# Optimization experiments

Hardware: AMD Instinct MI355X
Metric: run time of the kernel (lower is better)

The kernel has to match this reference:

```python
import jax, jax.numpy as jnp
import numpy as np

N, E, D, L = 100000, 500000, 128, 5
NUM_ATOM_FEATS, ATOM_VOCAB = 9, 120
NUM_BOND_FEATS, BOND_VOCAB = 3, 8
BN_EPS = 1e-5


def setup_inputs() -> dict:
    key = jax.random.key(0)
    ks = jax.random.split(key, 16)
    inp = {
        "x": jax.random.randint(ks[0], (N, NUM_ATOM_FEATS), 0, ATOM_VOCAB),
        "edge_index": jax.random.randint(ks[1], (2, E), 0, N),
        "edge_attr": jax.random.randint(ks[2], (E, NUM_BOND_FEATS), 0, BOND_VOCAB),
        "edge_weight": jax.random.uniform(ks[3], (E,), dtype=jnp.float32),
        # parameters
        "atom_emb": jax.random.normal(ks[4], (NUM_ATOM_FEATS, ATOM_VOCAB, D), dtype=jnp.float32) * 0.02,
        "bond_emb": jax.random.normal(ks[5], (L, NUM_BOND_FEATS, BOND_VOCAB, D), dtype=jnp.float32) * 0.02,
        "eps": jnp.zeros((L,), dtype=jnp.float32),
        "W1": jax.random.normal(ks[6], (L, D, 2 * D), dtype=jnp.float32) / np.sqrt(D),
        "b1": jnp.zeros((L, 2 * D), dtype=jnp.float32),
        "g1": jnp.ones((L, 2 * D), dtype=jnp.float32),
        "bt1": jnp.zeros((L, 2 * D), dtype=jnp.float32),
        "W2": jax.random.normal(ks[7], (L, 2 * D, D), dtype=jnp.float32) / np.sqrt(2 * D),
        "b2": jnp.zeros((L, D), dtype=jnp.float32),
        "g_out": jnp.ones((L, D), dtype=jnp.float32),
        "bt_out": jnp.zeros((L, D), dtype=jnp.float32),
    }
    return inp


def _batchnorm(h, g, b):
    # training-mode BN over node axis, biased variance (matches torch BN normalization)
    mu = jnp.mean(h, axis=0)
    var = jnp.mean((h - mu) ** 2, axis=0)
    return g * (h - mu) * jax.lax.rsqrt(var + BN_EPS) + b


def reference(x, edge_index, edge_attr, edge_weight,
              atom_emb, bond_emb, eps, W1, b1, g1, bt1, W2, b2, g_out, bt_out):
    # AtomEncoder: sum per-column embedding lookups -> [N, D]
    h = atom_emb[jnp.arange(NUM_ATOM_FEATS)[None, :], x].sum(axis=1)
    src, dst = edge_index[0], edge_index[1]
    ew = edge_weight[:, None]
    for l in range(L):
        # BondEncoder for layer l -> [E, D]
        e = bond_emb[l][jnp.arange(NUM_BOND_FEATS)[None, :], edge_attr].sum(axis=1)
        # message: relu(x_j + edge_emb) * edge_weight ; aggregate: scatter-add at dst
        m = jax.nn.relu(h[src] + e) * ew
        agg = jax.ops.segment_sum(m, dst, num_segments=N)
        z = (1.0 + eps[l]) * h + agg
        # GIN MLP: Linear -> BN -> ReLU -> Linear
        z = jax.nn.relu(_batchnorm(z @ W1[l] + b1[l], g1[l], bt1[l])) @ W2[l] + b2[l]
        # outer BatchNorm; dropout is identity in eval mode
        h_new = _batchnorm(z, g_out[l], bt_out[l])
        h = h_new if l == L - 1 else jax.nn.relu(h_new)
    return h
```

## Files before the change

### kernel.cpp

```cpp
#include <hip/hip_runtime.h>
#include <hip/hip_bf16.h>
#include <hip/hip_fp16.h>

#define NN 100000
#define EE 500000
#define NP 100096

typedef _Float16 f16;
typedef __attribute__((ext_vector_type(8))) _Float16 f16x8;
typedef __attribute__((ext_vector_type(4))) _Float16 f16x4;
typedef __attribute__((ext_vector_type(4))) float f32x4;

static __device__ __forceinline__ f16x8 relu8(f16x8 a) {
#if __has_builtin(__builtin_elementwise_max)
  f16x8 z = {0, 0, 0, 0, 0, 0, 0, 0};
  return __builtin_elementwise_max(a, z);
#else
  f16x8 r;
#pragma unroll
  for (int i = 0; i < 8; ++i) r[i] = (a[i] > (f16)0) ? a[i] : (f16)0;
  return r;
#endif
}

__global__ __launch_bounds__(256) void init_kernel(const float* __restrict__ W1,
                                                   const float* __restrict__ W2,
                                                   f16* __restrict__ w1f,
                                                   f16* __restrict__ w2f,
                                                   int* __restrict__ deg,
                                                   float* __restrict__ slices,
                                                   int* __restrict__ dmeta) {
  int gid = blockIdx.x * 256 + threadIdx.x;
  if (gid < 163840) {
    int l = gid / 32768; int rem = gid % 32768;
    int k = rem / 256;   int n = rem % 256;
    int ctg = n >> 4, m = n & 15;
    int c = k >> 5, q = (k >> 3) & 3, e = k & 7;
    int lane = q * 16 + m;
    w1f[l * 32768 + ((ctg * 4 + c) * 64 + lane) * 8 + e] = (f16)W1[gid];
  } else if (gid < 327680) {
    int g = gid - 163840;
    int l = g / 32768; int rem = g % 32768;
    int k = rem / 128; int n = rem % 128;
    int ctg = n >> 4, m = n & 15;
    int c = k >> 5, q = (k >> 3) & 3, e = k & 7;
    int lane = q * 16 + m;
    w2f[l * 32768 + ((ctg * 8 + c) * 64 + lane) * 8 + e] = (f16)W2[g];
  } else if (gid < 427680) {
    int i = gid - 327680;
    if (i < NN) deg[i] = 0;
  } else if (gid < 439968) {
    slices[gid - 427680] = 0.f;
  } else if (gid < 440096) {
    dmeta[gid - 439968] = 0;
  }
}

__global__ __launch_bounds__(256) void bondtab_kernel(const float* __restrict__ bemb,
                                                      f16* __restrict__ tab) {
  int gid = blockIdx.x * 256 + threadIdx.x;
  int l = gid >> 16;
  int rem = gid & 65535;
  int combo = rem >> 7, d = rem & 127;
  int a0 = combo & 7, a1 = (combo >> 3) & 7, a2 = combo >> 6;
  const float* bl = bemb + l * 3072;
  float v = bl[a0 * 128 + d] + bl[1024 + a1 * 128 + d] + bl[2048 + a2 * 128 + d];
  tab[gid] = (f16)v;
}

__global__ __launch_bounds__(256) void hist_kernel(const int* __restrict__ ei, int* __restrict__ deg) {
  int e = blockIdx.x * 256 + threadIdx.x;
  if (e < EE) atomicAdd(&deg[ei[EE + e]], 1);
}

__global__ __launch_bounds__(256) void scan1_kernel(const int* __restrict__ deg,
                                                    int* __restrict__ offs,
                                                    int* __restrict__ bsum) {
  __shared__ int sh[256];
  int b = blockIdx.x, t = threadIdx.x;
  int base = b * 1024 + t * 4;
  int v[4];
  int s = 0;
#pragma unroll
  for (int i = 0; i < 4; ++i) { v[i] = (base + i < NN) ? deg[base + i] : 0; s += v[i]; }
  sh[t] = s;
  __syncthreads();
  for (int off = 1; off < 256; off <<= 1) {
    int x = (t >= off) ? sh[t - off] : 0;
    __syncthreads();
    sh[t] += x;
    __syncthreads();
  }
  int excl = sh[t] - s;
  if (t == 255) bsum[b] = sh[255];
  int run = excl;
#pragma unroll
  for (int i = 0; i < 4; ++i) {
    if (base + i < NN) offs[base + i] = run;
    run += v[i];
  }
}

__global__ void scan2_kernel(int* __restrict__ bsum, int nb) {
  if (threadIdx.x == 0 && blockIdx.x == 0) {
    int run = 0;
    for (int i = 0; i < nb; ++i) { int v = bsum[i]; bsum[i] = run; run += v; }
  }
}

__global__ __launch_bounds__(256) void scan3_kernel(int* __restrict__ offs,
                                                    const int* __restrict__ bsum,
                                                    int* __restrict__ cursor) {
  int i = blockIdx.x * 256 + threadIdx.x;
  if (i < NN) {
    int v = offs[i] + bsum[i >> 10];
    offs[i] = v;
    cursor[i] = v;
  } else if (i == NN) {
    offs[NN] = EE;
  }
}

__global__ __launch_bounds__(256) void scatter_kernel(const int* __restrict__ ei,
                                                      const int* __restrict__ ea,
                                                      const float* __restrict__ ew,
                                                      int* __restrict__ cursor,
                                                      int2* __restrict__ pkw) {
  int e = blockIdx.x * 256 + threadIdx.x;
  if (e >= EE) return;
  int dst = ei[EE + e];
  int pos = atomicAdd(&cursor[dst], 1);
  int src = ei[e];
  int a0 = ea[e * 3 + 0], a1 = ea[e * 3 + 1], a2 = ea[e * 3 + 2];
  pkw[pos] = make_int2(src | (a0 << 17) | (a1 << 20) | (a2 << 23), __float_as_int(ew[e]));
}

__global__ __launch_bounds__(256) void dhist_kernel(const int* __restrict__ deg,
                                                    int* __restrict__ dhist) {
  __shared__ int lh[64];
  int t = threadIdx.x;
  if (t < 64) lh[t] = 0;
  __syncthreads();
  int n = blockIdx.x * 256 + t;
  if (n < NN) {
    int d = deg[n]; if (d > 63) d = 63;
    atomicAdd(&lh[d], 1);
  }
  __syncthreads();
  if (t < 64 && lh[t] > 0) atomicAdd(&dhist[t], lh[t]);
}

__global__ void dscan_kernel(const int* __restrict__ dhist, int* __restrict__ dcur) {
  if (threadIdx.x == 0 && blockIdx.x == 0) {
    int run = 0;
    for (int i = 0; i < 64; ++i) { int v = dhist[i]; dcur[i] = run; run += v; }
  }
}

__global__ __launch_bounds__(256) void dscatter_kernel(const int* __restrict__ deg,
                                                       int* __restrict__ dcur,
                                                       int* __restrict__ norder) {
  __shared__ int lcnt[64], lbase[64];
  int t = threadIdx.x;
  if (t < 64) lcnt[t] = 0;
  __syncthreads();
  int n = blockIdx.x * 256 + t;
  int b = 0, lpos = 0;
  bool valid = (n < NN);
  if (valid) {
    b = deg[n]; if (b > 63) b = 63;
    lpos = atomicAdd(&lcnt[b], 1);
  }
  __syncthreads();
  if (t < 64 && lcnt[t] > 0) lbase[t] = atomicAdd(&dcur[t], lcnt[t]);
  __syncthreads();
  if (valid) norder[lbase[b] + lpos] = n;
}

__global__ __launch_bounds__(256) void atom_kernel(const int* __restrict__ x,
                                                   const float* __restrict__ aemb,
                                                   f16* __restrict__ hf) {
  int gid = blockIdx.x * 256 + threadIdx.x;
  int n = gid >> 5, qq = gid & 31;
  if (n >= NN) return;
  float4 s = {0.f, 0.f, 0.f, 0.f};
#pragma unroll
  for (int f = 0; f < 9; ++f) {
    int xi = x[n * 9 + f];
    float4 v = *(const float4*)(aemb + (f * 120 + xi) * 128 + qq * 4);
    s.x += v.x; s.y += v.y; s.z += v.z; s.w += v.w;
  }
  f16x4 o;
  o[0] = (f16)s.x; o[1] = (f16)s.y; o[2] = (f16)s.z; o[3] = (f16)s.w;
  *(f16x4*)(hf + (long)n * 128 + qq * 4) = o;
}

__global__ __launch_bounds__(256) void edge_agg_kernel(const int* __restrict__ offs,
                                                       const int2* __restrict__ pkw,
                                                       const f16* __restrict__ tab,
                                                       const float* __restrict__ eps,
                                                       const int* __restrict__ norder,
                                                       const f16* __restrict__ hf,
                                                       f16* __restrict__ zb) {
  int gid = blockIdx.x * 256 + threadIdx.x;
  int g = gid >> 4, d0 = (gid & 15) * 8;
  if (g >= NN) {
    f16x8 z = {0, 0, 0, 0, 0, 0, 0, 0};
    *(f16x8*)(zb + (long)g * 128 + d0) = z;
    return;
  }
  int n = norder[g];
  int s0 = offs[n], s1 = offs[n + 1];
  float e1 = 1.f + eps[0];
  f16x8 hn = *(const f16x8*)(hf + (long)n * 128 + d0);
  float acc[8];
#pragma unroll
  for (int i = 0; i < 8; ++i) acc[i] = e1 * (float)hn[i];

  float wA, wB; f16x8 hA, bA, hB, bB;
  if (s0 < s1) {
    int2 pw = pkw[s0]; wA = __int_as_float(pw.y);
    hA = *(const f16x8*)(hf + (long)(pw.x & 131071) * 128 + d0);
    bA = *(const f16x8*)(tab + ((pw.x >> 17) & 511) * 128 + d0);
  }
  if (s0 + 1 < s1) {
    int2 pw = pkw[s0 + 1]; wB = __int_as_float(pw.y);
    hB = *(const f16x8*)(hf + (long)(pw.x & 131071) * 128 + d0);
    bB = *(const f16x8*)(tab + ((pw.x >> 17) & 511) * 128 + d0);
  }
  int e = s0;
  for (; e + 1 < s1; e += 2) {
    {
      f16x8 sm = relu8(hA + bA);
#pragma unroll
      for (int i = 0; i < 8; ++i) acc[i] += (float)sm[i] * wA;
      if (e + 2 < s1) {
        int2 pw = pkw[e + 2]; wA = __int_as_float(pw.y);
        hA = *(const f16x8*)(hf + (long)(pw.x & 131071) * 128 + d0);
        bA = *(const f16x8*)(tab + ((pw.x >> 17) & 511) * 128 + d0);
      }
    }
    {
      f16x8 sm = relu8(hB + bB);
#pragma unroll
      for (int i = 0; i < 8; ++i) acc[i] += (float)sm[i] * wB;
      if (e + 3 < s1) {
        int2 pw = pkw[e + 3]; wB = __int_as_float(pw.y);
        hB = *(const f16x8*)(hf + (long)(pw.x & 131071) * 128 + d0);
        bB = *(const f16x8*)(tab + ((pw.x >> 17) & 511) * 128 + d0);
      }
    }
  }
  if (e < s1) {
    f16x8 sm = relu8(hA + bA);
#pragma unroll
    for (int i = 0; i < 8; ++i) acc[i] += (float)sm[i] * wA;
  }
  f16x8 o;
#pragma unroll
  for (int i = 0; i < 8; ++i) o[i] = (f16)acc[i];
  *(f16x8*)(zb + (long)n * 128 + d0) = o;
}

__global__ __launch_bounds__(256) void edge_agg_bn_kernel(const int* __restrict__ offs,
                                                          const int2* __restrict__ pkw,
                                                          const f16* __restrict__ tab,
                                                          const float* __restrict__ eps, int l,
                                                          const int* __restrict__ norder,
                                                          const f16* __restrict__ t2,
                                                          const float* __restrict__ sum2s,
                                                          const float* __restrict__ sq2s,
                                                          const float* __restrict__ g2,
                                                          const float* __restrict__ bt2,
                                                          float* __restrict__ s1z,
                                                          f16* __restrict__ zb) {
  __shared__ float sc2[128], sh2[128];
  const int tid = threadIdx.x;
  if (tid < 128) {
    float s = 0.f, s2 = 0.f;
#pragma unroll
    for (int k = 0; k < 16; ++k) { s += sum2s[k * 128 + tid]; s2 += sq2s[k * 128 + tid]; }
    float mu = s * (1.f / NN);
    float var = fmaxf(s2 * (1.f / NN) - mu * mu, 0.f);
    float is = rsqrtf(var + 1e-5f);
    float sc = g2[tid] * is;
    sc2[tid] = sc;
    sh2[tid] = bt2[tid] - mu * sc;
  }
  if (blockIdx.x == 0) {
#pragma unroll
    for (int j = 0; j < 8; ++j)
      *(float4*)(s1z + (j * 256 + tid) * 4) = float4{0.f, 0.f, 0.f, 0.f};
  }
  __syncthreads();
  int gid = blockIdx.x * 256 + tid;
  int g = gid >> 4, d0 = (gid & 15) * 8;
  if (g >= NN) {
    f16x8 z = {0, 0, 0, 0, 0, 0, 0, 0};
    *(f16x8*)(zb + (long)g * 128 + d0) = z;
    return;
  }
  int n = norder[g];
  float4 svA = *(const float4*)(sc2 + d0), svB = *(const float4*)(sc2 + d0 + 4);
  float4 shA = *(const float4*)(sh2 + d0), shB = *(const float4*)(sh2 + d0 + 4);
  float sv[8] = {svA.x, svA.y, svA.z, svA.w, svB.x, svB.y, svB.z, svB.w};
  float hv[8] = {shA.x, shA.y, shA.z, shA.w, shB.x, shB.y, shB.z, shB.w};
  f16x8 sv8, hv8;
#pragma unroll
  for (int i = 0; i < 8; ++i) { sv8[i] = (f16)sv[i]; hv8[i] = (f16)hv[i]; }

  int s0 = offs[n], s1 = offs[n + 1];
  float e1 = 1.f + eps[l];
  f16x8 hn = *(const f16x8*)(t2 + (long)n * 128 + d0);
  float acc[8];
#pragma unroll
  for (int i = 0; i < 8; ++i)
    acc[i] = e1 * fmaxf((float)hn[i] * sv[i] + hv[i], 0.f);

  float wA, wB; f16x8 hA, bA, hB, bB;
  if (s0 < s1) {
    int2 pw = pkw[s0]; wA = __int_as_float(pw.y);
    hA = *(const f16x8*)(t2 + (long)(pw.x & 131071) * 128 + d0);
    bA = *(const f16x8*)(tab + ((pw.x >> 17) & 511) * 128 + d0);
  }
  if (s0 + 1 < s1) {
    int2 pw = pkw[s0 + 1]; wB = __int_as_float(pw.y);
    hB = *(const f16x8*)(t2 + (long)(pw.x & 131071) * 128 + d0);
    bB = *(const f16x8*)(tab + ((pw.x >> 17) & 511) * 128 + d0);
  }
  int e = s0;
  for (; e + 1 < s1; e += 2) {
    {
      f16x8 y = relu8(hA * sv8 + hv8);
      f16x8 sm = relu8(y + bA);
#pragma unroll
      for (int i = 0; i < 8; ++i) acc[i] += (float)sm[i] * wA;
      if (e + 2 < s1) {
        int2 pw = pkw[e + 2]; wA = __int_as_float(pw.y);
        hA = *(const f16x8*)(t2 + (long)(pw.x & 131071) * 128 + d0);
        bA = *(const f16x8*)(tab + ((pw.x >> 17) & 511) * 128 + d0);
      }
    }
    {
      f16x8 y = relu8(hB * sv8 + hv8);
      f16x8 sm = relu8(y + bB);
#pragma unroll
      for (int i = 0; i < 8; ++i) acc[i] += (float)sm[i] * wB;
      if (e + 3 < s1) {
        int2 pw = pkw[e + 3]; wB = __int_as_float(pw.y);
        hB = *(const f16x8*)(t2 + (long)(pw.x & 131071) * 128 + d0);
        bB = *(const f16x8*)(tab + ((pw.x >> 17) & 511) * 128 + d0);
      }
    }
  }
  if (e < s1) {
    f16x8 y = relu8(hA * sv8 + hv8);
    f16x8 sm = relu8(y + bA);
#pragma unroll
    for (int i = 0; i < 8; ++i) acc[i] += (float)sm[i] * wA;
  }
  f16x8 o;
#pragma unroll
  for (int i = 0; i < 8; ++i) o[i] = (f16)acc[i];
  *(f16x8*)(zb + (long)n * 128 + d0) = o;
}

__global__ __launch_bounds__(256) void gemm1_kernel(const f16* __restrict__ zb,
                                                    const f16* __restrict__ w1f,
                                                    f16* __restrict__ t1f,
                                                    float* __restrict__ sum1s,
                                                    float* __restrict__ sq1s,
                                                    float* __restrict__ s2z) {
  __shared__ __align__(16) char ldsraw[17408];
  const int tid = threadIdx.x;
  const int lane = tid & 63, w = tid >> 6;
  const int wr = w >> 1, wc = w & 1;
  const int m = lane & 15, q = lane >> 4;
  const int cb = blockIdx.x;
  const int rbase = blockIdx.y * 64;
  const int slice = blockIdx.y & 15;

  if (blockIdx.y == 0 && cb == 0) {
#pragma unroll
    for (int j = 0; j < 4; ++j)
      *(float4*)(s2z + (j * 256 + tid) * 4) = float4{0.f, 0.f, 0.f, 0.f};
  }

  f16x8 B[4][4];
#pragma unroll
  for (int ct = 0; ct < 4; ++ct)
#pragma unroll
    for (int c = 0; c < 4; ++c)
      B[ct][c] = *(const f16x8*)(w1f + (((cb * 8 + wc * 4 + ct) * 4 + c) * 64 + lane) * 8);

  {
    f16x8 st[4];
    const int tofs = tid * 16;
#pragma unroll
    for (int j = 0; j < 4; ++j)
      st[j] = *(const f16x8*)(zb + (long)rbase * 128 + (tofs + j * 4096) / 2);
#pragma unroll
    for (int j = 0; j < 4; ++j) {
      int ofs = tofs + j * 4096;
      int row = ofs >> 8, colb = ofs & 255;
      *(f16x8*)(ldsraw + row * 256 + (colb ^ ((row & 7) << 4))) = st[j];
    }
  }
  __syncthreads();

  f16x8 A[2][4];
#pragma unroll
  for (int rt = 0; rt < 2; ++rt) {
    int row = wr * 32 + rt * 16 + m;
    int rs = row * 256, sw = (row & 7) << 4;
#pragma unroll
    for (int c = 0; c < 4; ++c) {
      int colb = c * 64 + q * 16;
      A[rt][c] = *(const f16x8*)(ldsraw + rs + (colb ^ sw));
    }
  }

  f32x4 acc[2][4];
  const f32x4 zf = {0.f, 0.f, 0.f, 0.f};
#pragma unroll
  for (int a = 0; a < 2; ++a)
#pragma unroll
    for (int b = 0; b < 4; ++b) acc[a][b] = zf;

#pragma unroll
  for (int c = 0; c < 4; ++c)
#pragma unroll
    for (int rt = 0; rt < 2; ++rt)
#pragma unroll
      for (int ct = 0; ct < 4; ++ct)
        acc[rt][ct] = __builtin_amdgcn_mfma_f32_16x16x32_f16(A[rt][c], B[ct][c], acc[rt][ct], 0, 0, 0);

  __syncthreads();
  f16 (*sh)[136] = (f16(*)[136])ldsraw;

#pragma unroll
  for (int ct = 0; ct < 4; ++ct) {
    int lc = wc * 64 + ct * 16 + m;
    int gc = cb * 128 + lc;
    float s = 0.f, s2 = 0.f;
#pragma unroll
    for (int rt = 0; rt < 2; ++rt) {
      int lr = wr * 32 + rt * 16 + q * 4;
#pragma unroll
      for (int i = 0; i < 4; ++i) {
        float v = acc[rt][ct][i];
        s += v; s2 += v * v;
        sh[lr + i][lc] = (f16)v;
      }
    }
    s  += __shfl_xor(s, 16);  s  += __shfl_xor(s, 32);
    s2 += __shfl_xor(s2, 16); s2 += __shfl_xor(s2, 32);
    if (q == 0) {
      unsafeAtomicAdd(&sum1s[slice * 256 + gc], s);
      unsafeAtomicAdd(&sq1s[slice * 256 + gc], s2);
    }
  }
  __syncthreads();
  const int colc = tid & 15, r0 = tid >> 4;
#pragma unroll
  for (int j = 0; j < 4; ++j) {
    int r = j * 16 + r0;
    f16x8 v = *(const f16x8*)(&sh[r][colc * 8]);
    *(f16x8*)(t1f + (long)(rbase + r) * 256 + cb * 128 + colc * 8) = v;
  }
}

__global__ __launch_bounds__(256) void gemm2_kernel(const f16* __restrict__ a1,
                                                    const f16* __restrict__ w2f,
                                                    const float* __restrict__ sum1s,
                                                    const float* __restrict__ sq1s,
                                                    const float* __restrict__ g1,
                                                    const float* __restrict__ bt1,
                                                    f16* __restrict__ t2out,
                                                    float* __restrict__ sum2s,
                                                    float* __restrict__ sq2s) {
  __shared__ __align__(16) char ldsraw[34816];
  float* sc1 = (float*)(ldsraw + 32768);
  float* sh1 = (float*)(ldsraw + 33792);
  const int tid = threadIdx.x;
  const int lane = tid & 63, w = tid >> 6;
  const int wr = w >> 1, wc = w & 1;
  const int m = lane & 15, q = lane >> 4;
  const int rbase = blockIdx.x * 64;
  const int slice = blockIdx.x & 15;

  f16x8 st[8];
  const int tofs = tid * 16;
#pragma unroll
  for (int j = 0; j < 8; ++j)
    st[j] = *(const f16x8*)(a1 + (long)rbase * 256 + (tofs + j * 4096) / 2);

  {
    float s = 0.f, s2 = 0.f;
#pragma unroll
    for (int k = 0; k < 16; ++k) { s += sum1s[k * 256 + tid]; s2 += sq1s[k * 256 + tid]; }
    float mu = s * (1.f / NN);
    float var = fmaxf(s2 * (1.f / NN) - mu * mu, 0.f);
    float is = rsqrtf(var + 1e-5f);
    float sc = g1[tid] * is;
    sc1[tid] = sc;
    sh1[tid] = bt1[tid] - mu * sc;
  }
  __syncthreads();

  {
    const int k0 = (tid & 31) * 8;
    float4 sa = *(const float4*)(sc1 + k0);
    float4 sb = *(const float4*)(sc1 + k0 + 4);
    float4 ha = *(const float4*)(sh1 + k0);
    float4 hb = *(const float4*)(sh1 + k0 + 4);
#pragma unroll
    for (int j = 0; j < 8; ++j) {
      int ofs = tofs + j * 4096;
      int row = ofs >> 9, colb = ofs & 511;
      f16x8 u = st[j], o;
      o[0] = (f16)fmaxf((float)u[0] * sa.x + ha.x, 0.f);
      o[1] = (f16)fmaxf((float)u[1] * sa.y + ha.y, 0.f);
      o[2] = (f16)fmaxf((float)u[2] * sa.z + ha.z, 0.f);
      o[3] = (f16)fmaxf((float)u[3] * sa.w + ha.w, 0.f);
      o[4] = (f16)fmaxf((float)u[4] * sb.x + hb.x, 0.f);
      o[5] = (f16)fmaxf((float)u[5] * sb.y + hb.y, 0.f);
      o[6] = (f16)fmaxf((float)u[6] * sb.z + hb.z, 0.f);
      o[7] = (f16)fmaxf((float)u[7] * sb.w + hb.w, 0.f);
      *(f16x8*)(ldsraw + row * 512 + (colb ^ ((row & 7) << 4))) = o;
    }
  }
  __syncthreads();

  f32x4 acc[2][4];
  const f32x4 zf = {0.f, 0.f, 0.f, 0.f};
#pragma unroll
  for (int a = 0; a < 2; ++a)
#pragma unroll
    for (int b = 0; b < 4; ++b) acc[a][b] = zf;

#pragma unroll
  for (int hh = 0; hh < 2; ++hh) {
    f16x8 A[2][4], B[4][4];
#pragma unroll
    for (int rt = 0; rt < 2; ++rt) {
      int row = wr * 32 + rt * 16 + m;
      int rs = row * 512, sw = (row & 7) << 4;
#pragma unroll
      for (int c = 0; c < 4; ++c) {
        int colb = (hh * 4 + c) * 64 + q * 16;
        A[rt][c] = *(const f16x8*)(ldsraw + rs + (colb ^ sw));
      }
    }
#pragma unroll
    for (int ct = 0; ct < 4; ++ct)
#pragma unroll
      for (int c = 0; c < 4; ++c)
        B[ct][c] = *(const f16x8*)(w2f + (((wc * 4 + ct) * 8 + hh * 4 + c) * 64 + lane) * 8);
#pragma unroll
    for (int c = 0; c < 4; ++c)
#pragma unroll
      for (int rt = 0; rt < 2; ++rt)
#pragma unroll
        for (int ct = 0; ct < 4; ++ct)
          acc[rt][ct] = __builtin_amdgcn_mfma_f32_16x16x32_f16(A[rt][c], B[ct][c], acc[rt][ct], 0, 0, 0);
  }

  __syncthreads();
  f16 (*sh)[136] = (f16(*)[136])ldsraw;

#pragma unroll
  for (int ct = 0; ct < 4; ++ct) {
    int gc = wc * 64 + ct * 16 + m;
    float s = 0.f, s2 = 0.f;
#pragma unroll
    for (int rt = 0; rt < 2; ++rt) {
      int grow = rbase + wr * 32 + rt * 16 + q * 4;
      int lr = wr * 32 + rt * 16 + q * 4;
#pragma unroll
      for (int i = 0; i < 4; ++i) {
        float v = acc[rt][ct][i];
        float vv = (grow + i < NN) ? v : 0.f;
        s += vv; s2 += vv * vv;
        sh[lr + i][gc] = (f16)v;
      }
    }
    s  += __shfl_xor(s, 16);  s  += __shfl_xor(s, 32);
    s2 += __shfl_xor(s2, 16); s2 += __shfl_xor(s2, 32);
    if (q == 0) {
      unsafeAtomicAdd(&sum2s[slice * 128 + gc], s);
      unsafeAtomicAdd(&sq2s[slice * 128 + gc], s2);
    }
  }
  __syncthreads();
  const int colc = tid & 15, r0 = tid >> 4;
#pragma unroll
  for (int j = 0; j < 4; ++j) {
    int r = j * 16 + r0;
    f16x8 v = *(const f16x8*)(&sh[r][colc * 8]);
    *(f16x8*)(t2out + (long)(rbase + r) * 128 + colc * 8) = v;
  }
}

__global__ __launch_bounds__(256) void apply_kernel(const f16* __restrict__ t2,
                                                    const float* __restrict__ sum2s,
                                                    const float* __restrict__ sq2s,
                                                    const float* __restrict__ g2,
                                                    const float* __restrict__ bt2,
                                                    float* __restrict__ outp) {
  __shared__ float sc2[128], sh2[128];
  const int tid = threadIdx.x;
  if (tid < 128) {
    float s = 0.f, s2 = 0.f;
#pragma unroll
    for (int k = 0; k < 16; ++k) { s += sum2s[k * 128 + tid]; s2 += sq2s[k * 128 + tid]; }
    float mu = s * (1.f / NN);
    float var = fmaxf(s2 * (1.f / NN) - mu * mu, 0.f);
    float is = rsqrtf(var + 1e-5f);
    float sc = g2[tid] * is;
    sc2[tid] = sc;
    sh2[tid] = bt2[tid] - mu * sc;
  }
  __syncthreads();
  const int rbase = blockIdx.x * 64;
#pragma unroll
  for (int k = 0; k < 4; ++k) {
    int ci = tid + k * 256;
    int r = ci >> 4, c8 = ci & 15;
    int row = rbase + r;
    if (row >= NN) continue;
    f16x8 u = *(const f16x8*)(t2 + (long)row * 128 + c8 * 8);
    float4 sa = *(const float4*)(sc2 + c8 * 8);
    float4 sb = *(const float4*)(sc2 + c8 * 8 + 4);
    float4 ha = *(const float4*)(sh2 + c8 * 8);
    float4 hb = *(const float4*)(sh2 + c8 * 8 + 4);
    float4 o0 = {(float)u[0] * sa.x + ha.x, (float)u[1] * sa.y + ha.y,
                 (float)u[2] * sa.z + ha.z, (float)u[3] * sa.w + ha.w};
    float4 o1 = {(float)u[4] * sb.x + hb.x, (float)u[5] * sb.y + hb.y,
                 (float)u[6] * sb.z + hb.z, (float)u[7] * sb.w + hb.w};
    *(float4*)(outp + (long)row * 128 + c8 * 8) = o0;
    *(float4*)(outp + (long)row * 128 + c8 * 8 + 4) = o1;
  }
}

extern "C" void kernel_launch(void* const* d_in, const int* in_sizes, int n_in,
                              void* d_out, int out_size, void* d_ws, size_t ws_size,
                              hipStream_t stream) {
  (void)in_sizes; (void)n_in; (void)out_size; (void)ws_size;
  const int*   x      = (const int*)d_in[0];
  const int*   ei     = (const int*)d_in[1];
  const int*   ea     = (const int*)d_in[2];
  const float* ew     = (const float*)d_in[3];
  const float* aemb   = (const float*)d_in[4];
  const float* bemb   = (const float*)d_in[5];
  const float* eps    = (const float*)d_in[6];
  const float* W1     = (const float*)d_in[7];
  const float* g1     = (const float*)d_in[9];
  const float* bt1    = (const float*)d_in[10];
  const float* W2     = (const float*)d_in[11];
  const float* g_out  = (const float*)d_in[13];
  const float* bt_out = (const float*)d_in[14];

  float* outp = (float*)d_out;

  char* ws = (char*)d_ws;
  f16*   hf    = (f16*)(ws);
  f16*   zb    = (f16*)(ws + 25624576);
  f16*   t1f   = (f16*)(ws + 51249152);
  f16*   w1f   = (f16*)(ws + 102498304);
  f16*   w2f   = (f16*)(ws + 102825984);
  float* slices= (float*)(ws + 103153664);
  int*   offs  = (int*)(ws + 103202816);
  int*   bsum  = (int*)(ws + 103602848);
  int*   deg   = (int*)(ws + 103603360);
  int*   cursor= (int*)(ws + 104003360);
  f16*   bsumtab = (f16*)(ws + 103603360);
  int2*  pkw   = (int2*)(ws + 104403360);
  int*   norder= (int*)(ws + 108403360);
  int*   dmeta = (int*)(ws + 108803744);

  int* dhist = dmeta;
  int* dcur  = dmeta + 64;

  float* sum1s = slices;
  float* sq1s  = slices + 4096;
  float* sum2s = slices + 8192;
  float* sq2s  = slices + 10240;

  init_kernel<<<1720, 256, 0, stream>>>(W1, W2, w1f, w2f, deg, slices, dmeta);
  hist_kernel<<<1954, 256, 0, stream>>>(ei, deg);
  scan1_kernel<<<98, 256, 0, stream>>>(deg, offs, bsum);
  scan2_kernel<<<1, 64, 0, stream>>>(bsum, 98);
  scan3_kernel<<<392, 256, 0, stream>>>(offs, bsum, cursor);
  scatter_kernel<<<1954, 256, 0, stream>>>(ei, ea, ew, cursor, pkw);
  dhist_kernel<<<391, 256, 0, stream>>>(deg, dhist);
  dscan_kernel<<<1, 64, 0, stream>>>(dhist, dcur);
  dscatter_kernel<<<391, 256, 0, stream>>>(deg, dcur, norder);
  bondtab_kernel<<<1280, 256, 0, stream>>>(bemb, bsumtab);
  atom_kernel<<<12500, 256, 0, stream>>>(x, aemb, hf);

  for (int l = 0; l < 5; ++l) {
    if (l == 0) {
      edge_agg_kernel<<<6256, 256, 0, stream>>>(offs, pkw, bsumtab, eps, norder, hf, zb);
    } else {
      edge_agg_bn_kernel<<<6256, 256, 0, stream>>>(offs, pkw, bsumtab + l * 65536, eps, l,
                                                   norder, hf, sum2s, sq2s,
                                                   g_out + (l - 1) * 128, bt_out + (l - 1) * 128,
                                                   sum1s, zb);
    }
    gemm1_kernel<<<dim3(2, 1564), 256, 0, stream>>>(zb, w1f + l * 32768, t1f, sum1s, sq1s, sum2s);
    gemm2_kernel<<<1564, 256, 0, stream>>>(t1f, w2f + l * 32768, sum1s, sq1s,
                                           g1 + l * 256, bt1 + l * 256, hf, sum2s, sq2s);
    if (l == 4)
      apply_kernel<<<1564, 256, 0, stream>>>(hf, sum2s, sq2s, g_out + 512, bt_out + 512, outp);
  }
}
```

Before: 588.9 us.

## Fuse GIN MLP GEMMs into one persistent kernel with grid barrier

```diff
diff --git a/kernel.cpp b/kernel.cpp
--- a/kernel.cpp
+++ b/kernel.cpp
@@ -5,6 +5,8 @@
 #define NN 100000
 #define EE 500000
 #define NP 100096
+#define NTILE 1564
+#define NBLK 782
 
 typedef _Float16 f16;
 typedef __attribute__((ext_vector_type(8))) _Float16 f16x8;
@@ -51,7 +53,7 @@
     if (i < NN) deg[i] = 0;
   } else if (gid < 439968) {
     slices[gid - 427680] = 0.f;
-  } else if (gid < 440096) {
+  } else if (gid < 440104) {
     dmeta[gid - 439968] = 0;
   }
 }
@@ -365,135 +367,194 @@
   *(f16x8*)(zb + (long)n * 128 + d0) = o;
 }
 
-__global__ __launch_bounds__(256) void gemm1_kernel(const f16* __restrict__ zb,
-                                                    const f16* __restrict__ w1f,
-                                                    f16* __restrict__ t1f,
-                                                    float* __restrict__ sum1s,
-                                                    float* __restrict__ sq1s,
-                                                    float* __restrict__ s2z) {
-  __shared__ __align__(16) char ldsraw[17408];
+__device__ __forceinline__ void phaseA(int tile, const f16* __restrict__ zb,
+                                       const f16* __restrict__ w1f,
+                                       float* __restrict__ sum1s, float* __restrict__ sq1s,
+                                       char* lds, f16x8 (&H)[2][2][2]) {
   const int tid = threadIdx.x;
   const int lane = tid & 63, w = tid >> 6;
   const int wr = w >> 1, wc = w & 1;
   const int m = lane & 15, q = lane >> 4;
-  const int cb = blockIdx.x;
-  const int rbase = blockIdx.y * 64;
-  const int slice = blockIdx.y & 15;
-
-  if (blockIdx.y == 0 && cb == 0) {
-#pragma unroll
-    for (int j = 0; j < 4; ++j)
-      *(float4*)(s2z + (j * 256 + tid) * 4) = float4{0.f, 0.f, 0.f, 0.f};
-  }
-
-  f16x8 B[4][4];
-#pragma unroll
-  for (int ct = 0; ct < 4; ++ct)
-#pragma unroll
-    for (int c = 0; c < 4; ++c)
-      B[ct][c] = *(const f16x8*)(w1f + (((cb * 8 + wc * 4 + ct) * 4 + c) * 64 + lane) * 8);
-
-  {
-    f16x8 st[4];
-    const int tofs = tid * 16;
-#pragma unroll
-    for (int j = 0; j < 4; ++j)
-      st[j] = *(const f16x8*)(zb + (long)rbase * 128 + (tofs + j * 4096) / 2);
-#pragma unroll
-    for (int j = 0; j < 4; ++j) {
-      int ofs = tofs + j * 4096;
-      int row = ofs >> 8, colb = ofs & 255;
-      *(f16x8*)(ldsraw + row * 256 + (colb ^ ((row & 7) << 4))) = st[j];
-    }
-  }
-  __syncthreads();
-
-  f16x8 A[2][4];
-#pragma unroll
-  for (int rt = 0; rt < 2; ++rt) {
-    int row = wr * 32 + rt * 16 + m;
-    int rs = row * 256, sw = (row & 7) << 4;
+  const long rbase = (long)tile * 64;
+  const int slice = tile & 15;
+  f16x8 st[4];
+  const int tofs = tid * 16;
+#pragma unroll
+  for (int j = 0; j < 4; ++j)
+    st[j] = *(const f16x8*)(zb + rbase * 128 + (tofs + j * 4096) / 2);
+  __syncthreads();
+#pragma unroll
+  for (int j = 0; j < 4; ++j) {
+    int ofs = tofs + j * 4096;
+    int row = ofs >> 8, colb = ofs & 255;
+    *(f16x8*)(lds + row * 256 + (colb ^ ((row & 7) << 4))) = st[j];
+  }
+  __syncthreads();
+  const int r0 = wr * 32 + m, r1 = wr * 32 + 16 + m;
+  const int sw = (m & 7) << 4;
+#pragma unroll
+  for (int h = 0; h < 2; ++h) {
+    f32x4 a0c[4], a1c[4];
+    const f32x4 zf = {0.f, 0.f, 0.f, 0.f};
+#pragma unroll
+    for (int ct = 0; ct < 4; ++ct) { a0c[ct] = zf; a1c[ct] = zf; }
 #pragma unroll
     for (int c = 0; c < 4; ++c) {
       int colb = c * 64 + q * 16;
-      A[rt][c] = *(const f16x8*)(ldsraw + rs + (colb ^ sw));
-    }
-  }
-
-  f32x4 acc[2][4];
-  const f32x4 zf = {0.f, 0.f, 0.f, 0.f};
-#pragma unroll
-  for (int a = 0; a < 2; ++a)
-#pragma unroll
-    for (int b = 0; b < 4; ++b) acc[a][b] = zf;
-
-#pragma unroll
-  for (int c = 0; c < 4; ++c)
-#pragma unroll
-    for (int rt = 0; rt < 2; ++rt)
-#pragma unroll
-      for (int ct = 0; ct < 4; ++ct)
-        acc[rt][ct] = __builtin_amdgcn_mfma_f32_16x16x32_f16(A[rt][c], B[ct][c], acc[rt][ct], 0, 0, 0);
-
-  __syncthreads();
-  f16 (*sh)[136] = (f16(*)[136])ldsraw;
-
-#pragma unroll
-  for (int ct = 0; ct < 4; ++ct) {
-    int lc = wc * 64 + ct * 16 + m;
-    int gc = cb * 128 + lc;
-    float s = 0.f, s2 = 0.f;
-#pragma unroll
-    for (int rt = 0; rt < 2; ++rt) {
-      int lr = wr * 32 + rt * 16 + q * 4;
+      f16x8 A0 = *(const f16x8*)(lds + r0 * 256 + (colb ^ sw));
+      f16x8 A1 = *(const f16x8*)(lds + r1 * 256 + (colb ^ sw));
+#pragma unroll
+      for (int ct = 0; ct < 4; ++ct) {
+        f16x8 B = *(const f16x8*)(w1f + (((h * 8 + wc * 4 + ct) * 4 + c) * 64 + lane) * 8);
+        a0c[ct] = __builtin_amdgcn_mfma_f32_16x16x32_f16(A0, B, a0c[ct], 0, 0, 0);
+        a1c[ct] = __builtin_amdgcn_mfma_f32_16x16x32_f16(A1, B, a1c[ct], 0, 0, 0);
+      }
+    }
+#pragma unroll
+    for (int ct = 0; ct < 4; ++ct) {
+      int gc = h * 128 + wc * 64 + ct * 16 + m;
+      float s = 0.f, s2 = 0.f;
 #pragma unroll
       for (int i = 0; i < 4; ++i) {
-        float v = acc[rt][ct][i];
-        s += v; s2 += v * v;
-        sh[lr + i][lc] = (f16)v;
-      }
-    }
-    s  += __shfl_xor(s, 16);  s  += __shfl_xor(s, 32);
-    s2 += __shfl_xor(s2, 16); s2 += __shfl_xor(s2, 32);
-    if (q == 0) {
-      unsafeAtomicAdd(&sum1s[slice * 256 + gc], s);
-      unsafeAtomicAdd(&sq1s[slice * 256 + gc], s2);
-    }
-  }
-  __syncthreads();
-  const int colc = tid & 15, r0 = tid >> 4;
-#pragma unroll
-  for (int j = 0; j < 4; ++j) {
-    int r = j * 16 + r0;
-    f16x8 v = *(const f16x8*)(&sh[r][colc * 8]);
-    *(f16x8*)(t1f + (long)(rbase + r) * 256 + cb * 128 + colc * 8) = v;
-  }
-}
-
-__global__ __launch_bounds__(256) void gemm2_kernel(const f16* __restrict__ a1,
-                                                    const f16* __restrict__ w2f,
-                                                    const float* __restrict__ sum1s,
-                                                    const float* __restrict__ sq1s,
-                                                    const float* __restrict__ g1,
-                                                    const float* __restrict__ bt1,
-                                                    f16* __restrict__ t2out,
-                                                    float* __restrict__ sum2s,
-                                                    float* __restrict__ sq2s) {
-  __shared__ __align__(16) char ldsraw[34816];
-  float* sc1 = (float*)(ldsraw + 32768);
-  float* sh1 = (float*)(ldsraw + 33792);
+        float v0 = a0c[ct][i], v1 = a1c[ct][i];
+        s += v0 + v1; s2 += v0 * v0 + v1 * v1;
+        H[h][0][(ct * 4 + i) >> 3][(ct * 4 + i) & 7] = (f16)v0;
+        H[h][1][(ct * 4 + i) >> 3][(ct * 4 + i) & 7] = (f16)v1;
+      }
+      s  += __shfl_xor(s, 16);  s  += __shfl_xor(s, 32);
+      s2 += __shfl_xor(s2, 16); s2 += __shfl_xor(s2, 32);
+      if (q == 0) {
+        unsafeAtomicAdd(&sum1s[slice * 256 + gc], s);
+        unsafeAtomicAdd(&sq1s[slice * 256 + gc], s2);
+      }
+    }
+  }
+}
+
+__device__ __forceinline__ void phaseB(int tile, const f16* __restrict__ w2f,
+                                       const float* scL, const float* shL,
+                                       float* __restrict__ sum2s, float* __restrict__ sq2s,
+                                       f16* __restrict__ t2out,
+                                       char* lds, f16x8 (&H)[2][2][2]) {
   const int tid = threadIdx.x;
   const int lane = tid & 63, w = tid >> 6;
   const int wr = w >> 1, wc = w & 1;
   const int m = lane & 15, q = lane >> 4;
-  const int rbase = blockIdx.x * 64;
-  const int slice = blockIdx.x & 15;
-
-  f16x8 st[8];
-  const int tofs = tid * 16;
-#pragma unroll
-  for (int j = 0; j < 8; ++j)
-    st[j] = *(const f16x8*)(a1 + (long)rbase * 256 + (tofs + j * 4096) / 2);
+  const long rbase = (long)tile * 64;
+  const int slice = tile & 15;
+  const int r0 = wr * 32 + m, r1 = wr * 32 + 16 + m;
+  const int sw = (m & 7) << 4;
+  f32x4 o0c[4], o1c[4];
+  const f32x4 zf = {0.f, 0.f, 0.f, 0.f};
+#pragma unroll
+  for (int ct = 0; ct < 4; ++ct) { o0c[ct] = zf; o1c[ct] = zf; }
+#pragma unroll
+  for (int h = 0; h < 2; ++h) {
+#pragma unroll
+    for (int rt = 0; rt < 2; ++rt) {
+#pragma unroll
+      for (int ct = 0; ct < 4; ++ct) {
+        int lc = wc * 64 + ct * 16 + m;
+        int gc = h * 128 + lc;
+        float sc = scL[gc], sh = shL[gc];
+#pragma unroll
+        for (int i = 0; i < 4; ++i) {
+          float v = (float)H[h][rt][(ct * 4 + i) >> 3][(ct * 4 + i) & 7];
+          int r = wr * 32 + rt * 16 + q * 4 + i;
+          *(f16*)(lds + r * 256 + ((2 * lc) ^ ((r & 7) << 4))) = (f16)fmaxf(v * sc + sh, 0.f);
+        }
+      }
+    }
+    __syncthreads();
+#pragma unroll
+    for (int c = 0; c < 4; ++c) {
+      int colb = c * 64 + q * 16;
+      f16x8 A0 = *(const f16x8*)(lds + r0 * 256 + (colb ^ sw));
+      f16x8 A1 = *(const f16x8*)(lds + r1 * 256 + (colb ^ sw));
+#pragma unroll
+      for (int ct = 0; ct < 4; ++ct) {
+        f16x8 B = *(const f16x8*)(w2f + (((wc * 4 + ct) * 8 + h * 4 + c) * 64 + lane) * 8);
+        o0c[ct] = __builtin_amdgcn_mfma_f32_16x16x32_f16(A0, B, o0c[ct], 0, 0, 0);
+        o1c[ct] = __builtin_amdgcn_mfma_f32_16x16x32_f16(A1, B, o1c[ct], 0, 0, 0);
+      }
+    }
+    __syncthreads();
+  }
+  f16 (*sh136)[136] = (f16(*)[136])lds;
+#pragma unroll
+  for (int ct = 0; ct < 4; ++ct) {
+    int gc = wc * 64 + ct * 16 + m;
+    float s = 0.f, s2 = 0.f;
+    long grow0 = rbase + wr * 32 + q * 4;
+    long grow1 = grow0 + 16;
+    int lr0 = wr * 32 + q * 4, lr1 = lr0 + 16;
+#pragma unroll
+    for (int i = 0; i < 4; ++i) {
+      float v = o0c[ct][i];
+      float vm = (grow0 + i < NN) ? v : 0.f;
+      s += vm; s2 += vm * vm;
+      sh136[lr0 + i][gc] = (f16)v;
+    }
+#pragma unroll
+    for (int i = 0; i < 4; ++i) {
+      float v = o1c[ct][i];
+      float vm = (grow1 + i < NN) ? v : 0.f;
+      s += vm; s2 += vm * vm;
+      sh136[lr1 + i][gc] = (f16)v;
+    }
+    s  += __shfl_xor(s, 16);  s  += __shfl_xor(s, 32);
+    s2 += __shfl_xor(s2, 16); s2 += __shfl_xor(s2, 32);
+    if (q == 0) {
+      unsafeAtomicAdd(&sum2s[slice * 128 + gc], s);
+      unsafeAtomicAdd(&sq2s[slice * 128 + gc], s2);
+    }
+  }
+  __syncthreads();
+  const int colc = tid & 15, rr = tid >> 4;
+#pragma unroll
+  for (int j = 0; j < 4; ++j) {
+    int r = j * 16 + rr;
+    f16x8 v = *(const f16x8*)(&sh136[r][colc * 8]);
+    *(f16x8*)(t2out + (rbase + r) * 128 + colc * 8) = v;
+  }
+  __syncthreads();
+}
+
+__global__ __launch_bounds__(256, 4) void gemm12_kernel(const f16* __restrict__ zb,
+                                                        const f16* __restrict__ w1f,
+                                                        const f16* __restrict__ w2f,
+                                                        const float* __restrict__ g1,
+                                                        const float* __restrict__ bt1,
+                                                        float* __restrict__ sum1s,
+                                                        float* __restrict__ sq1s,
+                                                        float* __restrict__ sum2s,
+                                                        f16* __restrict__ t2out,
+                                                        int* __restrict__ bar) {
+  __shared__ __align__(16) char lds[19456];
+  float* scL = (float*)(lds + 17408);
+  float* shL = (float*)(lds + 18432);
+  const int tid = threadIdx.x;
+  const int b = blockIdx.x;
+  const int t0v = 2 * b, t1v = 2 * b + 1;
+  f16x8 H0[2][2][2], H1[2][2][2];
+
+  if (b == 0) {
+#pragma unroll
+    for (int j = 0; j < 4; ++j)
+      *(float4*)(sum2s + (j * 256 + tid) * 4) = float4{0.f, 0.f, 0.f, 0.f};
+  }
+
+  phaseA(t0v, zb, w1f, sum1s, sq1s, lds, H0);
+  phaseA(t1v, zb, w1f, sum1s, sq1s, lds, H1);
+
+  __syncthreads();
+  if (tid == 0) {
+    __threadfence();
+    __hip_atomic_fetch_add(bar, 1, __ATOMIC_ACQ_REL, __HIP_MEMORY_SCOPE_AGENT);
+    while (__hip_atomic_load(bar, __ATOMIC_ACQUIRE, __HIP_MEMORY_SCOPE_AGENT) < NBLK)
+      __builtin_amdgcn_s_sleep(32);
+  }
+  __syncthreads();
 
   {
     float s = 0.f, s2 = 0.f;
@@ -503,103 +564,14 @@
     float var = fmaxf(s2 * (1.f / NN) - mu * mu, 0.f);
     float is = rsqrtf(var + 1e-5f);
     float sc = g1[tid] * is;
-    sc1[tid] = sc;
-    sh1[tid] = bt1[tid] - mu * sc;
-  }
-  __syncthreads();
-
-  {
-    const int k0 = (tid & 31) * 8;
-    float4 sa = *(const float4*)(sc1 + k0);
-    float4 sb = *(const float4*)(sc1 + k0 + 4);
-    float4 ha = *(const float4*)(sh1 + k0);
-    float4 hb = *(const float4*)(sh1 + k0 + 4);
-#pragma unroll
-    for (int j = 0; j < 8; ++j) {
-      int ofs = tofs + j * 4096;
-      int row = ofs >> 9, colb = ofs & 511;
-      f16x8 u = st[j], o;
-      o[0] = (f16)fmaxf((float)u[0] * sa.x + ha.x, 0.f);
-      o[1] = (f16)fmaxf((float)u[1] * sa.y + ha.y, 0.f);
-      o[2] = (f16)fmaxf((float)u[2] * sa.z + ha.z, 0.f);
-      o[3] = (f16)fmaxf((float)u[3] * sa.w + ha.w, 0.f);
-      o[4] = (f16)fmaxf((float)u[4] * sb.x + hb.x, 0.f);
-      o[5] = (f16)fmaxf((float)u[5] * sb.y + hb.y, 0.f);
-      o[6] = (f16)fmaxf((float)u[6] * sb.z + hb.z, 0.f);
-      o[7] = (f16)fmaxf((float)u[7] * sb.w + hb.w, 0.f);
-      *(f16x8*)(ldsraw + row * 512 + (colb ^ ((row & 7) << 4))) = o;
-    }
-  }
-  __syncthreads();
-
-  f32x4 acc[2][4];
-  const f32x4 zf = {0.f, 0.f, 0.f, 0.f};
-#pragma unroll
-  for (int a = 0; a < 2; ++a)
-#pragma unroll
-    for (int b = 0; b < 4; ++b) acc[a][b] = zf;
-
-#pragma unroll
-  for (int hh = 0; hh < 2; ++hh) {
-    f16x8 A[2][4], B[4][4];
-#pragma unroll
-    for (int rt = 0; rt < 2; ++rt) {
-      int row = wr * 32 + rt * 16 + m;
-      int rs = row * 512, sw = (row & 7) << 4;
-#pragma unroll
-      for (int c = 0; c < 4; ++c) {
-        int colb = (hh * 4 + c) * 64 + q * 16;
-        A[rt][c] = *(const f16x8*)(ldsraw + rs + (colb ^ sw));
-      }
-    }
-#pragma unroll
-    for (int ct = 0; ct < 4; ++ct)
-#pragma unroll
-      for (int c = 0; c < 4; ++c)
-        B[ct][c] = *(const f16x8*)(w2f + (((wc * 4 + ct) * 8 + hh * 4 + c) * 64 + lane) * 8);
-#pragma unroll
-    for (int c = 0; c < 4; ++c)
-#pragma unroll
-      for (int rt = 0; rt < 2; ++rt)
-#pragma unroll
-        for (int ct = 0; ct < 4; ++ct)
-          acc[rt][ct] = __builtin_amdgcn_mfma_f32_16x16x32_f16(A[rt][c], B[ct][c], acc[rt][ct], 0, 0, 0);
-  }
-
-  __syncthreads();
-  f16 (*sh)[136] = (f16(*)[136])ldsraw;
-
-#pragma unroll
-  for (int ct = 0; ct < 4; ++ct) {
-    int gc = wc * 64 + ct * 16 + m;
-    float s = 0.f, s2 = 0.f;
-#pragma unroll
-    for (int rt = 0; rt < 2; ++rt) {
-      int grow = rbase + wr * 32 + rt * 16 + q * 4;
-      int lr = wr * 32 + rt * 16 + q * 4;
-#pragma unroll
-      for (int i = 0; i < 4; ++i) {
-        float v = acc[rt][ct][i];
-        float vv = (grow + i < NN) ? v : 0.f;
-        s += vv; s2 += vv * vv;
-        sh[lr + i][gc] = (f16)v;
-      }
-    }
-    s  += __shfl_xor(s, 16);  s  += __shfl_xor(s, 32);
-    s2 += __shfl_xor(s2, 16); s2 += __shfl_xor(s2, 32);
-    if (q == 0) {
-      unsafeAtomicAdd(&sum2s[slice * 128 + gc], s);
-      unsafeAtomicAdd(&sq2s[slice * 128 + gc], s2);
-    }
-  }
-  __syncthreads();
-  const int colc = tid & 15, r0 = tid >> 4;
-#pragma unroll
-  for (int j = 0; j < 4; ++j) {
-    int r = j * 16 + r0;
-    f16x8 v = *(const f16x8*)(&sh[r][colc * 8]);
-    *(f16x8*)(t2out + (long)(rbase + r) * 128 + colc * 8) = v;
-  }
+    scL[tid] = sc;
+    shL[tid] = bt1[tid] - mu * sc;
+  }
+  __syncthreads();
+
+  float* sq2s = sum2s + 2048;
+  phaseB(t0v, w2f, scL, shL, sum2s, sq2s, t2out, lds, H0);
+  phaseB(t1v, w2f, scL, shL, sum2s, sq2s, t2out, lds, H1);
 }
 
 __global__ __launch_bounds__(256) void apply_kernel(const f16* __restrict__ t2,
@@ -666,7 +638,6 @@
   char* ws = (char*)d_ws;
   f16*   hf    = (f16*)(ws);
   f16*   zb    = (f16*)(ws + 25624576);
-  f16*   t1f   = (f16*)(ws + 51249152);
   f16*   w1f   = (f16*)(ws + 102498304);
   f16*   w2f   = (f16*)(ws + 102825984);
   float* slices= (float*)(ws + 103153664);
@@ -681,6 +652,7 @@
 
   int* dhist = dmeta;
   int* dcur  = dmeta + 64;
+  int* bar   = dmeta + 128;
 
   float* sum1s = slices;
   float* sq1s  = slices + 4096;
@@ -708,9 +680,9 @@
                                                    g_out + (l - 1) * 128, bt_out + (l - 1) * 128,
                                                    sum1s, zb);
     }
-    gemm1_kernel<<<dim3(2, 1564), 256, 0, stream>>>(zb, w1f + l * 32768, t1f, sum1s, sq1s, sum2s);
-    gemm2_kernel<<<1564, 256, 0, stream>>>(t1f, w2f + l * 32768, sum1s, sq1s,
-                                           g1 + l * 256, bt1 + l * 256, hf, sum2s, sq2s);
+    gemm12_kernel<<<NBLK, 256, 0, stream>>>(zb, w1f + l * 32768, w2f + l * 32768,
+                                            g1 + l * 256, bt1 + l * 256,
+                                            sum1s, sq1s, sum2s, hf, bar + l);
     if (l == 4)
       apply_kernel<<<1564, 256, 0, stream>>>(hf, sum2s, sq2s, g_out + 512, bt_out + 512, outp);
   }
```

New measurement: 1.824 ms. 210% more time.
